# Kernel optimization log

Hardware: AMD Instinct MI355X
Metric: run time of the kernel (lower is better)

The kernel has to match this reference:

```python
import jax, jax.numpy as jnp
import numpy as np

B, T, D_TOKEN = 32, 2048, 1024
N_HEADS, D_HEAD = 16, 64


def setup_inputs() -> dict:
    key = jax.random.key(0)
    k1, k2, k3, k4 = jax.random.split(key, 4)
    scale = 1.0 / np.sqrt(D_TOKEN)
    return {
        "x": jax.random.normal(k1, (B, T, D_TOKEN), dtype=jnp.float32),
        # torch Linear weight layout: [out_features, in_features]
        "W_heads": jax.random.normal(k2, (N_HEADS, D_HEAD, D_TOKEN), dtype=jnp.float32) * scale,
        "W_proj": jax.random.normal(k3, (D_TOKEN, N_HEADS * D_HEAD), dtype=jnp.float32) * scale,
        "b_proj": jax.random.normal(k4, (D_TOKEN,), dtype=jnp.float32) * scale,
    }


def reference(x, W_heads, W_proj, b_proj):
    b, t, d = x.shape
    n, h, _ = W_heads.shape
    # per-head bias-free linear projections; concat along channel == reshape of stacked einsum
    heads = jnp.einsum('btd,nhd->btnh', x, W_heads).reshape(b, t, n * h)  # [b, t, N*d_head]
    # sum-pool over tokens ('b t c -> b c', 'sum')
    x_concat = heads.sum(axis=1)  # [b, N*d_head]
    # output projection (with bias)
    return x_concat @ W_proj.T + b_proj  # [b, d_token]
```

## Files before the change

kernel.cpp:

```cpp
#include <hip/hip_runtime.h>

#define B 32
#define T 2048
#define D 1024

constexpr int TCHUNK = 64;
constexpr int NTC    = T / TCHUNK;

__global__ __launch_bounds__(256) void reduce_tokens(const float* __restrict__ x,
                                                     float* __restrict__ s) {
    const int blk = blockIdx.x;
    const int b   = blk >> 5;
    const int tc  = blk & (NTC - 1);
    const int d4  = threadIdx.x * 4;

    const float* base = x + ((size_t)b * T + (size_t)tc * TCHUNK) * D + d4;

    float4 acc = make_float4(0.f, 0.f, 0.f, 0.f);
    #pragma unroll 8
    for (int t = 0; t < TCHUNK; ++t) {
        float4 v = *(const float4*)(base + (size_t)t * D);
        acc.x += v.x; acc.y += v.y; acc.z += v.z; acc.w += v.w;
    }

    float* sp = s + b * D + d4;
    atomicAdd(sp + 0, acc.x);
    atomicAdd(sp + 1, acc.y);
    atomicAdd(sp + 2, acc.z);
    atomicAdd(sp + 3, acc.w);
}

__global__ __launch_bounds__(256) void gemv32(const float* __restrict__ A,
                                              const float* __restrict__ W,
                                              const float* __restrict__ bias,
                                              float* __restrict__ out,
                                              int has_bias) {
    const int g    = blockIdx.x * 4 + (threadIdx.x >> 6);
    const int lane = threadIdx.x & 63;
    const int b    = g & (B - 1);
    const int c    = g >> 5;

    const float* a = A + (size_t)b * D;
    const float* w = W + (size_t)c * D;

    float acc = 0.f;
    #pragma unroll
    for (int k = 0; k < 4; ++k) {
        const int d = k * 256 + lane * 4;
        float4 av = *(const float4*)(a + d);
        float4 wv = *(const float4*)(w + d);
        acc += av.x * wv.x + av.y * wv.y + av.z * wv.z + av.w * wv.w;
    }

    #pragma unroll
    for (int off = 32; off > 0; off >>= 1)
        acc += __shfl_xor(acc, off, 64);

    if (lane == 0) {
        float r = acc;
        if (has_bias) r += bias[c];
        out[(size_t)b * D + c] = r;
    }
}

extern "C" void kernel_launch(void* const* d_in, const int* in_sizes, int n_in,
                              void* d_out, int out_size, void* d_ws, size_t ws_size,
                              hipStream_t stream) {
    const float* x  = (const float*)d_in[0];
    const float* Wh = (const float*)d_in[1];
    const float* Wp = (const float*)d_in[2];
    const float* bp = (const float*)d_in[3];
    float* out = (float*)d_out;

    float* s   = (float*)d_ws;
    float* tmp = s + B * D;

    hipMemsetAsync(s, 0, (size_t)B * D * sizeof(float), stream);

    reduce_tokens<<<B * NTC, 256, 0, stream>>>(x, s);
    gemv32<<<(B * D) / 4, 256, 0, stream>>>(s,   Wh, nullptr, tmp, 0);
    gemv32<<<(B * D) / 4, 256, 0, stream>>>(tmp, Wp, bp,      out, 1);
}
```

Before: 382.5 us.

## Replace atomic token reduction with two-pass partials and batch-4 GEMV reuse

The token sum no longer uses float atomics and a memset. Each chunk writes its partial sum to workspace, and a second kernel reduces the 32 partials per batch row. The GEMV now computes four batch rows per wavefront, so each weight row is loaded once for four outputs instead of four times. This adds a kernel launch and a 4 MB partial buffer round trip, and cuts total atomic traffic and weight reloads.

Result: no change. 381.0 us (-0.4%).

```diff
diff --git a/kernel.cpp b/kernel.cpp
--- a/kernel.cpp
+++ b/kernel.cpp
@@ -7,8 +7,8 @@
 constexpr int TCHUNK = 64;
 constexpr int NTC    = T / TCHUNK;
 
-__global__ __launch_bounds__(256) void reduce_tokens(const float* __restrict__ x,
-                                                     float* __restrict__ s) {
+__global__ __launch_bounds__(256) void reduce_tokens_partial(const float* __restrict__ x,
+                                                             float* __restrict__ p) {
     const int blk = blockIdx.x;
     const int b   = blk >> 5;
     const int tc  = blk & (NTC - 1);
@@ -23,43 +23,65 @@
         acc.x += v.x; acc.y += v.y; acc.z += v.z; acc.w += v.w;
     }
 
-    float* sp = s + b * D + d4;
-    atomicAdd(sp + 0, acc.x);
-    atomicAdd(sp + 1, acc.y);
-    atomicAdd(sp + 2, acc.z);
-    atomicAdd(sp + 3, acc.w);
+    *(float4*)(p + ((size_t)b * NTC + tc) * D + d4) = acc;
 }
 
-__global__ __launch_bounds__(256) void gemv32(const float* __restrict__ A,
-                                              const float* __restrict__ W,
-                                              const float* __restrict__ bias,
-                                              float* __restrict__ out,
-                                              int has_bias) {
+__global__ __launch_bounds__(256) void reduce_partials(const float* __restrict__ p,
+                                                       float* __restrict__ s) {
+    const int b = blockIdx.x >> 2;
+    const int d = (blockIdx.x & 3) * 256 + threadIdx.x;
+
+    const float* pp = p + (size_t)b * NTC * D + d;
+    float acc = 0.f;
+    #pragma unroll
+    for (int tc = 0; tc < NTC; ++tc)
+        acc += pp[(size_t)tc * D];
+    s[(size_t)b * D + d] = acc;
+}
+
+__global__ __launch_bounds__(256) void gemv_b4(const float* __restrict__ A,
+                                               const float* __restrict__ W,
+                                               const float* __restrict__ bias,
+                                               float* __restrict__ out,
+                                               int has_bias) {
     const int g    = blockIdx.x * 4 + (threadIdx.x >> 6);
     const int lane = threadIdx.x & 63;
-    const int b    = g & (B - 1);
-    const int c    = g >> 5;
+    const int b0   = (g & 7) * 4;
+    const int c    = g >> 3;
 
-    const float* a = A + (size_t)b * D;
-    const float* w = W + (size_t)c * D;
+    const float* w  = W + (size_t)c * D;
+    const float* a0 = A + (size_t)b0 * D;
 
-    float acc = 0.f;
+    float acc0 = 0.f, acc1 = 0.f, acc2 = 0.f, acc3 = 0.f;
     #pragma unroll
     for (int k = 0; k < 4; ++k) {
         const int d = k * 256 + lane * 4;
-        float4 av = *(const float4*)(a + d);
         float4 wv = *(const float4*)(w + d);
-        acc += av.x * wv.x + av.y * wv.y + av.z * wv.z + av.w * wv.w;
+        float4 a;
+        a = *(const float4*)(a0 + d);
+        acc0 += a.x * wv.x + a.y * wv.y + a.z * wv.z + a.w * wv.w;
+        a = *(const float4*)(a0 + D + d);
+        acc1 += a.x * wv.x + a.y * wv.y + a.z * wv.z + a.w * wv.w;
+        a = *(const float4*)(a0 + 2 * D + d);
+        acc2 += a.x * wv.x + a.y * wv.y + a.z * wv.z + a.w * wv.w;
+        a = *(const float4*)(a0 + 3 * D + d);
+        acc3 += a.x * wv.x + a.y * wv.y + a.z * wv.z + a.w * wv.w;
     }
 
     #pragma unroll
-    for (int off = 32; off > 0; off >>= 1)
-        acc += __shfl_xor(acc, off, 64);
+    for (int off = 32; off > 0; off >>= 1) {
+        acc0 += __shfl_xor(acc0, off, 64);
+        acc1 += __shfl_xor(acc1, off, 64);
+        acc2 += __shfl_xor(acc2, off, 64);
+        acc3 += __shfl_xor(acc3, off, 64);
+    }
 
     if (lane == 0) {
-        float r = acc;
-        if (has_bias) r += bias[c];
-        out[(size_t)b * D + c] = r;
+        const float bb = has_bias ? bias[c] : 0.f;
+        out[(size_t)(b0 + 0) * D + c] = acc0 + bb;
+        out[(size_t)(b0 + 1) * D + c] = acc1 + bb;
+        out[(size_t)(b0 + 2) * D + c] = acc2 + bb;
+        out[(size_t)(b0 + 3) * D + c] = acc3 + bb;
     }
 }
 
@@ -72,12 +94,12 @@
     const float* bp = (const float*)d_in[3];
     float* out = (float*)d_out;
 
-    float* s   = (float*)d_ws;
-    float* tmp = s + B * D;
+    float* p   = (float*)d_ws;
+    float* s   = p + (size_t)B * NTC * D;
+    float* tmp = s + (size_t)B * D;
 
-    hipMemsetAsync(s, 0, (size_t)B * D * sizeof(float), stream);
-
-    reduce_tokens<<<B * NTC, 256, 0, stream>>>(x, s);
-    gemv32<<<(B * D) / 4, 256, 0, stream>>>(s,   Wh, nullptr, tmp, 0);
-    gemv32<<<(B * D) / 4, 256, 0, stream>>>(tmp, Wp, bp,      out, 1);
+    reduce_tokens_partial<<<B * NTC, 256, 0, stream>>>(x, p);
+    reduce_partials<<<128, 256, 0, stream>>>(p, s);
+    gemv_b4<<<(B / 4) * D / 4, 256, 0, stream>>>(s,   Wh, nullptr, tmp, 0);
+    gemv_b4<<<(B / 4) * D / 4, 256, 0, stream>>>(tmp, Wp, bp,      out, 1);
 }
```
